# Kernel tuning notes

Hardware: AMD Instinct MI355X
Metric: run time of the kernel (lower is better)

## Reference

```python
import jax, jax.numpy as jnp
import numpy as np

D = 768
N_ATOM = 1000 + 1   # num_atom_templates + 1
N_BOND = 300 + 1    # num_bond_templates + 1


def setup_inputs() -> dict:
    key = jax.random.key(0)
    k1, k2, k3, k4, k5 = jax.random.split(key, 5)
    scale = 1.0 / np.sqrt(D)
    return {
        "input_states": jax.random.normal(k1, (8, 256, D), dtype=jnp.float32),
        "Wa": jax.random.normal(k2, (N_ATOM, D), dtype=jnp.float32) * scale,
        "ba": jax.random.normal(k3, (N_ATOM,), dtype=jnp.float32) * 0.01,
        "Wb": jax.random.normal(k4, (N_BOND, 2 * D), dtype=jnp.float32) * scale,
        "bb": jax.random.normal(k5, (N_BOND,), dtype=jnp.float32) * 0.01,
    }


def reference(input_states, Wa, ba, Wb, bb):
    # Atom head: [B, L, n_a]
    atom_logits = jnp.einsum("bld,ad->bla", input_states, Wa) + ba

    # Bond head. Original math: linear(cat(x_i, x_j)) over all pairs (i, j).
    # Since Linear(cat(x_i, x_j)) = x_i @ W1.T + x_j @ W2.T + b with
    # W1 = Wb[:, :D], W2 = Wb[:, D:], we project once per token and
    # broadcast-add, avoiding the O(L^2 * 2D) concat intermediate.
    W1 = Wb[:, :D]
    W2 = Wb[:, D:]
    p1 = jnp.einsum("bld,nd->bln", input_states, W1)  # [B, L, n_b]
    p2 = jnp.einsum("bld,nd->bln", input_states, W2)  # [B, L, n_b]
    bond_logits = p1[:, :, None, :] + p2[:, None, :, :] + bb  # [B, L, L, n_b]

    return (atom_logits, bond_logits)
```

## Files before the change

kernel.cpp:

```cpp
#include <hip/hip_runtime.h>

#define DK      768
#define M_ROWS  2048
#define N_ATOM  1001
#define N_BOND  301
#define N_TOT   1603
#define N_PADR  1664
#define ATOM_ELEMS 2050048
#define P_ELEMS    616448
#define SLAB_F4    19264

typedef __attribute__((ext_vector_type(4))) float f32x4;
typedef __attribute__((ext_vector_type(8))) short bf16x8;

static __device__ __forceinline__ unsigned short f2bf(float f) {
    unsigned u = __float_as_uint(f);
    u += 0x7FFFu + ((u >> 16) & 1u);
    return (unsigned short)(u >> 16);
}

static __device__ __forceinline__ void gload_lds16(const void* g, void* l) {
    __builtin_amdgcn_global_load_lds(
        (const __attribute__((address_space(1))) unsigned*)g,
        (__attribute__((address_space(3))) unsigned*)l, 16, 0, 0);
}

__global__ __launch_bounds__(256) void pack_bf16(
    const float* __restrict__ x, const float* __restrict__ Wa,
    const float* __restrict__ Wb,
    ushort* __restrict__ xb, ushort* __restrict__ wcat)
{
    const int NX4 = (M_ROWS * DK) / 4;
    const int NW4 = (N_PADR * DK) / 4;
    int t = blockIdx.x * 256 + threadIdx.x;
    if (t < NX4) {
        float4 v = ((const float4*)x)[t];
        ushort4 o;
        o.x = f2bf(v.x); o.y = f2bf(v.y); o.z = f2bf(v.z); o.w = f2bf(v.w);
        ((ushort4*)xb)[t] = o;
    } else if (t < NX4 + NW4) {
        int u = t - NX4;
        int r = u / 192;
        int c = (u - r * 192) * 4;
        float4 v = make_float4(0.f, 0.f, 0.f, 0.f);
        if (r < N_ATOM) {
            v = *(const float4*)(Wa + (size_t)r * DK + c);
        } else if (r < N_TOT) {
            int q = r - N_ATOM;
            v = *(const float4*)(Wb + (size_t)(q >> 1) * (2 * DK) + (q & 1) * DK + c);
        }
        ushort4 o;
        o.x = f2bf(v.x); o.y = f2bf(v.y); o.z = f2bf(v.z); o.w = f2bf(v.w);
        ((ushort4*)wcat)[u] = o;
    }
}

__global__ __launch_bounds__(256) void gemm_mfma(
    const ushort* __restrict__ xb, const ushort* __restrict__ wcat,
    const float* __restrict__ ba, const float* __restrict__ bb,
    float* __restrict__ atom, float* __restrict__ p1, float* __restrict__ p2)
{
    __shared__ char As[8192];
    __shared__ char Bs[8192];

    const int tid  = threadIdx.x;
    const int lane = tid & 63;
    const int wid  = tid >> 6;
    const int wr   = wid >> 1;
    const int wc   = wid & 1;
    const int m0   = blockIdx.y * 64;
    const int n0   = blockIdx.x * 64;

    f32x4 acc[2][2] = {};

    const int lrow = lane >> 3;
    const int lcx  = ((lane & 7) ^ lrow) * 8;

    const ushort* Ag = xb   + (size_t)m0 * DK;
    const ushort* Bg = wcat + (size_t)n0 * DK;

    for (int k0 = 0; k0 < DK; k0 += 64) {
        __syncthreads();
        #pragma unroll
        for (int t = 0; t < 2; ++t) {
            const int s = wid + 4 * t;
            gload_lds16(Ag + (size_t)(s * 8 + lrow) * DK + k0 + lcx, As + s * 1024);
            gload_lds16(Bg + (size_t)(s * 8 + lrow) * DK + k0 + lcx, Bs + s * 1024);
        }
        __syncthreads();
        #pragma unroll
        for (int ks = 0; ks < 2; ++ks) {
            const int kc = ks * 4 + (lane >> 4);
            bf16x8 af[2], bfr[2];
            #pragma unroll
            for (int i = 0; i < 2; ++i) {
                int ra = wr * 32 + i * 16 + (lane & 15);
                af[i]  = *(const bf16x8*)(As + ra * 128 + ((kc ^ (ra & 7)) << 4));
                int rb = wc * 32 + i * 16 + (lane & 15);
                bfr[i] = *(const bf16x8*)(Bs + rb * 128 + ((kc ^ (rb & 7)) << 4));
            }
            #pragma unroll
            for (int i = 0; i < 2; ++i)
                #pragma unroll
                for (int j = 0; j < 2; ++j)
                    acc[i][j] = __builtin_amdgcn_mfma_f32_16x16x32_bf16(
                        af[i], bfr[j], acc[i][j], 0, 0, 0);
        }
    }

    #pragma unroll
    for (int i = 0; i < 2; ++i) {
        #pragma unroll
        for (int j = 0; j < 2; ++j) {
            #pragma unroll
            for (int reg = 0; reg < 4; ++reg) {
                int m = m0 + wr * 32 + i * 16 + (lane >> 4) * 4 + reg;
                int n = n0 + wc * 32 + j * 16 + (lane & 15);
                float v = acc[i][j][reg];
                if (n < N_ATOM) {
                    atom[(size_t)m * N_ATOM + n] = v + ba[n];
                } else if (n < N_TOT) {
                    int q = n - N_ATOM, rr = q >> 1;
                    if (q & 1) p2[(size_t)m * N_BOND + rr] = v + bb[rr];
                    else       p1[(size_t)m * N_BOND + rr] = v;
                }
            }
        }
    }
}

__global__ __launch_bounds__(256) void bond_bcast(
    const float* __restrict__ p1, const float* __restrict__ p2,
    f32x4* __restrict__ out)
{
    __shared__ float p1s[344];
    const int bi  = blockIdx.x;
    const int b   = bi >> 8;
    const int tid = threadIdx.x;

    for (int n = tid; n < N_BOND; n += 256)
        p1s[n + (n >> 3)] = p1[(size_t)bi * N_BOND + n];
    __syncthreads();

    const f32x4* p2f = (const f32x4*)(p2 + (size_t)(b << 8) * N_BOND);
    f32x4* of = out + (size_t)bi * SLAB_F4;

    int n = (4 * tid) % 301;
    for (int f = tid; f < SLAB_F4; f += 256) {
        f32x4 v = p2f[f];
        int n0 = n;
        int n1 = n + 1; if (n1 >= 301) n1 -= 301;
        int n2 = n + 2; if (n2 >= 301) n2 -= 301;
        int n3 = n + 3; if (n3 >= 301) n3 -= 301;
        v.x += p1s[n0 + (n0 >> 3)];
        v.y += p1s[n1 + (n1 >> 3)];
        v.z += p1s[n2 + (n2 >> 3)];
        v.w += p1s[n3 + (n3 >> 3)];
        __builtin_nontemporal_store(v, &of[f]);
        n += 121; if (n >= 301) n -= 301;
    }
}

extern "C" void kernel_launch(void* const* d_in, const int* in_sizes, int n_in,
                              void* d_out, int out_size, void* d_ws, size_t ws_size,
                              hipStream_t stream) {
    const float* x  = (const float*)d_in[0];
    const float* Wa = (const float*)d_in[1];
    const float* ba = (const float*)d_in[2];
    const float* Wb = (const float*)d_in[3];
    const float* bb = (const float*)d_in[4];

    float* out  = (float*)d_out;
    float* atom = out;
    float* bond = out + ATOM_ELEMS;

    ushort* xb   = (ushort*)d_ws;
    ushort* wcat = xb + (size_t)M_ROWS * DK;
    float*  p1   = (float*)(wcat + (size_t)N_PADR * DK);
    float*  p2   = p1 + P_ELEMS;

    pack_bf16<<<dim3(2784), dim3(256), 0, stream>>>(x, Wa, Wb, xb, wcat);

    gemm_mfma<<<dim3(N_PADR / 64, M_ROWS / 64), dim3(256), 0, stream>>>(
        xb, wcat, ba, bb, atom, p1, p2);

    bond_bcast<<<dim3(2048), dim3(256), 0, stream>>>(p1, p2, (f32x4*)bond);
}
```

Before: 150.9 us.

## Double-buffer GEMM LDS tiles and restructure bond broadcast indexing and block order

The GEMM now double-buffers its A/B LDS tiles, prefetching the next K slice while the MFMAs run on the current one, and drops one barrier per iteration. Atom logits are written with nontemporal stores. The bond broadcast kernel stores a duplicated p1 row in LDS so the four-element window needs no modulo wraps, processes two float4s per loop trip, and permutes block indices so consecutive blocks hit different batches. These target load latency in the GEMM and index arithmetic in the store-bound broadcast, at the cost of twice the LDS and possible bank conflicts from dropping the padding.

```diff
diff --git a/kernel.cpp b/kernel.cpp
--- a/kernel.cpp
+++ b/kernel.cpp
@@ -60,8 +60,8 @@
     const float* __restrict__ ba, const float* __restrict__ bb,
     float* __restrict__ atom, float* __restrict__ p1, float* __restrict__ p2)
 {
-    __shared__ char As[8192];
-    __shared__ char Bs[8192];
+    __shared__ char As[2][8192];
+    __shared__ char Bs[2][8192];
 
     const int tid  = threadIdx.x;
     const int lane = tid & 63;
@@ -79,15 +79,15 @@
     const ushort* Ag = xb   + (size_t)m0 * DK;
     const ushort* Bg = wcat + (size_t)n0 * DK;
 
-    for (int k0 = 0; k0 < DK; k0 += 64) {
-        __syncthreads();
+    auto stage = [&](int buf, int k0) {
         #pragma unroll
         for (int t = 0; t < 2; ++t) {
             const int s = wid + 4 * t;
-            gload_lds16(Ag + (size_t)(s * 8 + lrow) * DK + k0 + lcx, As + s * 1024);
-            gload_lds16(Bg + (size_t)(s * 8 + lrow) * DK + k0 + lcx, Bs + s * 1024);
-        }
-        __syncthreads();
+            gload_lds16(Ag + (size_t)(s * 8 + lrow) * DK + k0 + lcx, &As[buf][s * 1024]);
+            gload_lds16(Bg + (size_t)(s * 8 + lrow) * DK + k0 + lcx, &Bs[buf][s * 1024]);
+        }
+    };
+    auto compute = [&](int buf) {
         #pragma unroll
         for (int ks = 0; ks < 2; ++ks) {
             const int kc = ks * 4 + (lane >> 4);
@@ -95,9 +95,9 @@
             #pragma unroll
             for (int i = 0; i < 2; ++i) {
                 int ra = wr * 32 + i * 16 + (lane & 15);
-                af[i]  = *(const bf16x8*)(As + ra * 128 + ((kc ^ (ra & 7)) << 4));
+                af[i]  = *(const bf16x8*)(&As[buf][ra * 128 + ((kc ^ (ra & 7)) << 4)]);
                 int rb = wc * 32 + i * 16 + (lane & 15);
-                bfr[i] = *(const bf16x8*)(Bs + rb * 128 + ((kc ^ (rb & 7)) << 4));
+                bfr[i] = *(const bf16x8*)(&Bs[buf][rb * 128 + ((kc ^ (rb & 7)) << 4)]);
             }
             #pragma unroll
             for (int i = 0; i < 2; ++i)
@@ -106,7 +106,17 @@
                     acc[i][j] = __builtin_amdgcn_mfma_f32_16x16x32_bf16(
                         af[i], bfr[j], acc[i][j], 0, 0, 0);
         }
-    }
+    };
+
+    stage(0, 0);
+    __syncthreads();
+    for (int t = 0; t < 11; ++t) {
+        const int cur = t & 1;
+        stage(cur ^ 1, (t + 1) * 64);
+        compute(cur);
+        __syncthreads();
+    }
+    compute(1);
 
     #pragma unroll
     for (int i = 0; i < 2; ++i) {
@@ -118,7 +128,7 @@
                 int n = n0 + wc * 32 + j * 16 + (lane & 15);
                 float v = acc[i][j][reg];
                 if (n < N_ATOM) {
-                    atom[(size_t)m * N_ATOM + n] = v + ba[n];
+                    __builtin_nontemporal_store(v + ba[n], &atom[(size_t)m * N_ATOM + n]);
                 } else if (n < N_TOT) {
                     int q = n - N_ATOM, rr = q >> 1;
                     if (q & 1) p2[(size_t)m * N_BOND + rr] = v + bb[rr];
@@ -133,31 +143,37 @@
     const float* __restrict__ p1, const float* __restrict__ p2,
     f32x4* __restrict__ out)
 {
-    __shared__ float p1s[344];
-    const int bi  = blockIdx.x;
+    __shared__ float p1s[608];
+    const int blk = blockIdx.x;
+    const int bi  = ((blk & 7) << 8) | (blk >> 3);
     const int b   = bi >> 8;
     const int tid = threadIdx.x;
 
-    for (int n = tid; n < N_BOND; n += 256)
-        p1s[n + (n >> 3)] = p1[(size_t)bi * N_BOND + n];
+    const float* row = p1 + (size_t)bi * N_BOND;
+    for (int k = tid; k < 604; k += 256)
+        p1s[k] = row[k >= N_BOND ? k - N_BOND : k];
     __syncthreads();
 
     const f32x4* p2f = (const f32x4*)(p2 + (size_t)(b << 8) * N_BOND);
     f32x4* of = out + (size_t)bi * SLAB_F4;
 
-    int n = (4 * tid) % 301;
-    for (int f = tid; f < SLAB_F4; f += 256) {
-        f32x4 v = p2f[f];
-        int n0 = n;
-        int n1 = n + 1; if (n1 >= 301) n1 -= 301;
-        int n2 = n + 2; if (n2 >= 301) n2 -= 301;
-        int n3 = n + 3; if (n3 >= 301) n3 -= 301;
-        v.x += p1s[n0 + (n0 >> 3)];
-        v.y += p1s[n1 + (n1 >> 3)];
-        v.z += p1s[n2 + (n2 >> 3)];
-        v.w += p1s[n3 + (n3 >> 3)];
-        __builtin_nontemporal_store(v, &of[f]);
-        n += 121; if (n >= 301) n -= 301;
+    int na = (4 * tid) % 301;
+    int nb = na + 121; if (nb >= 301) nb -= 301;
+
+    for (int f = tid; f < SLAB_F4; f += 512) {
+        {
+            f32x4 v = p2f[f];
+            v.x += p1s[na]; v.y += p1s[na + 1]; v.z += p1s[na + 2]; v.w += p1s[na + 3];
+            __builtin_nontemporal_store(v, &of[f]);
+        }
+        int f2 = f + 256;
+        if (f2 < SLAB_F4) {
+            f32x4 v = p2f[f2];
+            v.x += p1s[nb]; v.y += p1s[nb + 1]; v.z += p1s[nb + 2]; v.w += p1s[nb + 3];
+            __builtin_nontemporal_store(v, &of[f2]);
+        }
+        na += 242; if (na >= 301) na -= 301;
+        nb += 242; if (nb >= 301) nb -= 301;
     }
 }
 
```

Result: slower. 157.5 us (+4.4%).
